# Kernel tuning notes

Measured on AMD Instinct MI355X. Metric: run time of the kernel, lower is better.

Reference implementation:

```python
import jax, jax.numpy as jnp
import numpy as np

# MX microscaling decode helpers. Codes are stored as int32 holding uint8 bit patterns.
_FP4_MAG = jnp.array([0.0, 0.5, 1.0, 1.5, 2.0, 3.0, 4.0, 6.0], dtype=jnp.float32)  # E2M1

def dec_fp4(c):
    # c in [0,16): bit3 = sign, bits0-2 index E2M1 magnitude LUT
    s = jnp.where(c >= 8, -1.0, 1.0)
    return s * _FP4_MAG[c & 7]

def dec_fp6(c):
    # E3M2, bias 3. bit5 sign, bits2-4 exp, bits0-1 mantissa
    s = jnp.where(c >= 32, -1.0, 1.0)
    e = ((c >> 2) & 7).astype(jnp.float32)
    m = (c & 3).astype(jnp.float32)
    mag = jnp.where(e == 0, m * 0.25 * 0.25, (1.0 + m * 0.25) * jnp.exp2(e - 3.0))
    return s * mag

def dec_fp8(c):
    # E4M3, bias 7. bit7 sign, bits3-6 exp, bits0-2 mantissa (NaN code decoded as 480, consistent both sides)
    s = jnp.where(c >= 128, -1.0, 1.0)
    e = ((c >> 3) & 15).astype(jnp.float32)
    m = (c & 7).astype(jnp.float32)
    mag = jnp.where(e == 0, m * 0.125 * jnp.exp2(-6.0), (1.0 + m * 0.125) * jnp.exp2(e - 7.0))
    return s * mag

def unpack4(p):
    # [..., K//2] bytes -> [..., K] nibbles; low nibble = even element, high = odd
    lo = p & 15
    hi = (p >> 4) & 15
    return jnp.stack([lo, hi], axis=-1).reshape(*p.shape[:-1], p.shape[-1] * 2)

def unpack6(p):
    # little-endian 6-bit packing: 4 values per 3 bytes. [..., K*6//8] -> [..., K]
    g = p.reshape(*p.shape[:-1], -1, 3)
    b0, b1, b2 = g[..., 0], g[..., 1], g[..., 2]
    v0 = b0 & 0x3F
    v1 = ((b0 >> 6) & 3) | ((b1 & 0x0F) << 2)
    v2 = ((b1 >> 4) & 0x0F) | ((b2 & 3) << 4)
    v3 = (b2 >> 2) & 0x3F
    return jnp.stack([v0, v1, v2, v3], axis=-1).reshape(*p.shape[:-1], p.shape[-1] * 4 // 3)

def blockscale(x, sf):
    # x [..., K] fp32, sf [..., K//32] E8M0 exponents: scale = 2^(sf-127) per 32-element block
    scale = jnp.exp2(sf.astype(jnp.float32) - 127.0)
    xs = x.reshape(*x.shape[:-1], -1, 32) * scale[..., None]
    return xs.reshape(x.shape)

def dequant(codes, sf, bits):
    if bits == 4:
        x = dec_fp4(unpack4(codes))
    elif bits == 6:
        x = dec_fp6(unpack6(codes))
    else:
        x = dec_fp8(codes)
    return blockscale(x, sf)


def setup_inputs() -> dict:
    key = jax.random.key(0)
    ks = jax.random.split(key, 13)
    M, N = 4096, 4096
    p4, p6, p8 = 3072, 768, 256
    ri = lambda k, sh: jax.random.randint(k, sh, 0, 256, dtype=jnp.int32)
    sf = lambda k, sh: jax.random.randint(k, sh, 121, 132, dtype=jnp.int32)
    return {
        "AN": ri(ks[0], (M, p4 // 2)),
        "AS": ri(ks[1], (M, p6 * 6 // 8)),
        "AO": ri(ks[2], (M, p8)),
        "SFAN": sf(ks[3], (M, p4 // 32)),
        "SFAS": sf(ks[4], (M, p6 // 32)),
        "SFAO": sf(ks[5], (M, p8 // 32)),
        "BN": ri(ks[6], (N, p4 // 2)),
        "BS": ri(ks[7], (N, p6 * 6 // 8)),
        "BO": ri(ks[8], (N, p8)),
        "SFBN": sf(ks[9], (N * p4 // 32,)),
        "SFBS": sf(ks[10], (N * p6 // 32,)),
        "SFBO": sf(ks[11], (N * p8 // 32,)),
        "bias": jax.random.normal(ks[12], (N,), dtype=jnp.float32) * 0.02,
    }


def reference(AN, AS, AO, SFAN, SFAS, SFAO, BN, BS, BO, SFBN, SFBS, SFBO, bias):
    N = BN.shape[0]
    a4 = dequant(AN, SFAN, 4)                       # [M, p4]
    w4 = dequant(BN, SFBN.reshape(N, -1), 4)        # [N, p4]
    a6 = dequant(AS, SFAS, 6)                       # [M, p6]
    w6 = dequant(BS, SFBS.reshape(N, -1), 6)        # [N, p6]
    a8 = dequant(AO, SFAO, 8)                       # [M, p8]
    w8 = dequant(BO, SFBO.reshape(N, -1), 8)        # [N, p8]
    y = a4 @ w4.T + a6 @ w6.T + a8 @ w8.T           # [M, N]
    return y + bias
```

## Files before the change

kernel.cpp:

```cpp
#include <hip/hip_runtime.h>

typedef short short8 __attribute__((ext_vector_type(8)));
typedef int   intx8  __attribute__((ext_vector_type(8)));
typedef float floatx16 __attribute__((ext_vector_type(16)));

__device__ __forceinline__ unsigned pk4(int a, int b, int c, int d) {
    return (a & 255) | ((b & 255) << 8) | ((c & 255) << 16) | ((unsigned)(d & 255) << 24);
}

__device__ __forceinline__ unsigned dec8bf(int c, int esf) {
    int s = (c & 128) << 8;
    int e = (c >> 3) & 15, m = c & 7;
    int rn = s | ((e + 120 + esf) << 7) | (m << 4);
    int nb = (m >= 4) ? 2 : ((m >= 2) ? 1 : 0);
    int rs = m ? (s | ((nb + 118 + esf) << 7) | ((m << (7 - nb)) & 0x7F)) : s;
    return (unsigned)(e ? rn : rs);
}

__global__ __launch_bounds__(256) void pack_lds(
    const int* __restrict__ Pn, const int* __restrict__ Ps, const int* __restrict__ Po,
    const int* __restrict__ Sn, const int* __restrict__ Ss, const int* __restrict__ So,
    unsigned char* __restrict__ C4, unsigned char* __restrict__ C6,
    unsigned short* __restrict__ C8, unsigned char* __restrict__ St, int R)
{
    __shared__ unsigned lds[9216];
    int t = threadIdx.x, b = blockIdx.x, per = R >> 6;
    if (b < 4 * per) {
        int jg = b / per, rb = b - jg * per, r0 = rb << 6;
        #pragma unroll
        for (int i = 0; i < 24; ++i) {
            int idx = i * 256 + t, row = idx / 96, q4 = idx - row * 96;
            int4 v = *(const int4*)(Pn + (size_t)(r0 + row) * 1536 + jg * 384 + q4 * 4);
            lds[row * 96 + q4] = pk4(v.x, v.y, v.z, v.w);
        }
        __syncthreads();
        #pragma unroll
        for (int i = 0; i < 6; ++i) {
            int idx = i * 256 + t, j = idx >> 6, row = idx & 63;
            uint4 v = *(uint4*)&lds[row * 96 + j * 4];
            *(uint4*)(C4 + ((size_t)(jg * 24 + j) * R + r0 + row) * 16) = v;
        }
    } else if (b < 5 * per) {
        int rb = b - 4 * per, r0 = rb << 6;
        #pragma unroll
        for (int i = 0; i < 36; ++i) {
            int idx = i * 256 + t, row = idx / 144, q4 = idx - row * 144;
            int4 v = *(const int4*)(Ps + (size_t)(r0 + row) * 576 + q4 * 4);
            lds[row * 144 + q4] = pk4(v.x, v.y, v.z, v.w);
        }
        __syncthreads();
        #pragma unroll
        for (int i = 0; i < 18; ++i) {
            int idx = i * 256 + t, seg = idx / 192, off = idx - seg * 192;
            int row = off / 3, m3 = off - row * 3;
            int w0 = row * 144 + seg * 6 + m3 * 2;
            int2 v = { (int)lds[w0], (int)lds[w0 + 1] };
            *(int2*)(C6 + ((size_t)seg * R + r0) * 24 + (size_t)off * 8) = v;
        }
    } else if (b < 6 * per) {
        int rb = b - 5 * per, r0 = rb << 6;
        #pragma unroll
        for (int i = 0; i < 16; ++i) {
            int idx = i * 256 + t, row = idx >> 6, q4 = idx & 63;
            int4 c = *(const int4*)(Po + (size_t)(r0 + row) * 256 + q4 * 4);
            int e = So[(size_t)(r0 + row) * 8 + (q4 >> 3)] - 127;
            lds[row * 128 + q4 * 2]     = dec8bf(c.x & 255, e) | (dec8bf(c.y & 255, e) << 16);
            lds[row * 128 + q4 * 2 + 1] = dec8bf(c.z & 255, e) | (dec8bf(c.w & 255, e) << 16);
        }
        __syncthreads();
        #pragma unroll
        for (int i = 0; i < 8; ++i) {
            int idx = i * 256 + t, seg = idx >> 6, row = idx & 63;
            uint4 v = *(uint4*)&lds[row * 128 + seg * 4];
            *(uint4*)((unsigned char*)C8 + ((size_t)seg * R + r0 + row) * 16) = v;
        }
    } else if (b < 7 * per) {
        int rb = b - 6 * per, r0 = rb << 6;
        #pragma unroll
        for (int i = 0; i < 6; ++i) {
            int idx = i * 256 + t, row = idx / 24, q4 = idx - row * 24;
            int4 v = *(const int4*)(Sn + (size_t)(r0 + row) * 96 + q4 * 4);
            lds[row * 24 + q4] = pk4(v.x, v.y, v.z, v.w);
        }
        __syncthreads();
        #pragma unroll
        for (int i = 0; i < 6; ++i) {
            int idx = i * 256 + t, seg = idx >> 6, row = idx & 63;
            *(unsigned*)(St + ((size_t)seg * R + r0 + row) * 4) = lds[row * 24 + seg];
        }
    } else {
        int rb = b - 7 * per, r0 = rb << 6;
        #pragma unroll
        for (int i = 0; i < 3; ++i) {
            int idx = i * 256 + t, row = idx / 12, b2 = idx - row * 12;
            int2 v = *(const int2*)(Ss + (size_t)(r0 + row) * 24 + b2 * 2);
            lds[row * 12 + b2] = (unsigned)((v.x & 255) | ((v.y & 255) << 8));
        }
        __syncthreads();
        #pragma unroll
        for (int i = 0; i < 3; ++i) {
            int idx = i * 256 + t, seg = idx >> 6, row = idx & 63;
            *(unsigned*)(St + ((size_t)(24 + seg) * R + r0 + row) * 4) = lds[row * 12 + seg];
        }
    }
}

__global__ __launch_bounds__(256, 2) void gemm_mx(
    const unsigned char* __restrict__ A4, const unsigned char* __restrict__ B4,
    const unsigned char* __restrict__ A6, const unsigned char* __restrict__ B6,
    const unsigned short* __restrict__ A8, const unsigned short* __restrict__ B8,
    const unsigned char* __restrict__ SaT, const unsigned char* __restrict__ SbT,
    const float* __restrict__ bias, float* __restrict__ C, int M, int N)
{
    int tid = threadIdx.x, w = tid >> 6, l = tid & 63;
    int nbm = M >> 7, nbn = N >> 7;
    int bm, bn;
    if (nbm == 32 && nbn == 32) {
        int o = blockIdx.y * 32 + blockIdx.x;
        int xcd = o & 7, pos = o >> 3;
        int tile = pos >> 4, idx = pos & 15;
        bm = xcd * 4 + (idx & 3);
        bn = tile * 4 + (idx >> 2);
    } else { bm = blockIdx.y; bn = blockIdx.x; }

    int wm = (w >> 1) * 64, wn = (w & 1) * 64;
    int lr = l & 31, lh = l >> 5;

    floatx16 acc[2][2] = {};

    int rA[2] = { bm * 128 + wm + lr, bm * 128 + wm + 32 + lr };
    int cB[2] = { bn * 128 + wn + lr, bn * 128 + wn + 32 + lr };

    {
        unsigned strA = 32u * (unsigned)M, strB = 32u * (unsigned)N;
        unsigned fA0 = ((unsigned)lh * M + (unsigned)rA[0]) * 16u;
        unsigned fA1 = ((unsigned)lh * M + (unsigned)rA[1]) * 16u;
        unsigned fB0 = ((unsigned)lh * N + (unsigned)cB[0]) * 16u;
        unsigned fB1 = ((unsigned)lh * N + (unsigned)cB[1]) * 16u;

        int4 pa[4][2], pb[4][2];
        #pragma unroll
        for (int s = 0; s < 4; ++s) {
            pa[s][0] = *(const int4*)(A4 + fA0); pa[s][1] = *(const int4*)(A4 + fA1);
            pb[s][0] = *(const int4*)(B4 + fB0); pb[s][1] = *(const int4*)(B4 + fB1);
            fA0 += strA; fA1 += strA; fB0 += strB; fB1 += strB;
        }

        unsigned sstrA = 4u * (unsigned)M, sstrB = 4u * (unsigned)N;
        unsigned sA0 = (unsigned)rA[0] * 4u, sA1 = (unsigned)rA[1] * 4u;
        unsigned sB0 = (unsigned)cB[0] * 4u, sB1 = (unsigned)cB[1] * 4u;
        unsigned psa[2][2], psb[2][2];
        psa[0][0] = *(const unsigned*)(SaT + sA0);         psa[0][1] = *(const unsigned*)(SaT + sA1);
        psb[0][0] = *(const unsigned*)(SbT + sB0);         psb[0][1] = *(const unsigned*)(SbT + sB1);
        psa[1][0] = *(const unsigned*)(SaT + sA0 + sstrA); psa[1][1] = *(const unsigned*)(SaT + sA1 + sstrA);
        psb[1][0] = *(const unsigned*)(SbT + sB0 + sstrB); psb[1][1] = *(const unsigned*)(SbT + sB1 + sstrB);
        sA0 += 2 * sstrA; sA1 += 2 * sstrA; sB0 += 2 * sstrB; sB1 += 2 * sstrB;

        #pragma unroll 4
        for (int u = 0; u < 48; ++u) {
            int sl = u & 3, wsl = (u >> 1) & 1;
            int sh = 8 * ((u & 1) * 2 + lh);
            int sa0 = (int)((psa[wsl][0] >> sh) & 255), sa1 = (int)((psa[wsl][1] >> sh) & 255);
            int sb0 = (int)((psb[wsl][0] >> sh) & 255), sb1 = (int)((psb[wsl][1] >> sh) & 255);
            intx8 A0 = (intx8){ pa[sl][0].x, pa[sl][0].y, pa[sl][0].z, pa[sl][0].w, 0, 0, 0, 0 };
            intx8 A1 = (intx8){ pa[sl][1].x, pa[sl][1].y, pa[sl][1].z, pa[sl][1].w, 0, 0, 0, 0 };
            intx8 B0 = (intx8){ pb[sl][0].x, pb[sl][0].y, pb[sl][0].z, pb[sl][0].w, 0, 0, 0, 0 };
            intx8 B1 = (intx8){ pb[sl][1].x, pb[sl][1].y, pb[sl][1].z, pb[sl][1].w, 0, 0, 0, 0 };
            acc[0][0] = __builtin_amdgcn_mfma_scale_f32_32x32x64_f8f6f4(A0, B0, acc[0][0], 4, 4, 0, sa0, 0, sb0);
            acc[0][1] = __builtin_amdgcn_mfma_scale_f32_32x32x64_f8f6f4(A0, B1, acc[0][1], 4, 4, 0, sa0, 0, sb1);
            acc[1][0] = __builtin_amdgcn_mfma_scale_f32_32x32x64_f8f6f4(A1, B0, acc[1][0], 4, 4, 0, sa1, 0, sb0);
            acc[1][1] = __builtin_amdgcn_mfma_scale_f32_32x32x64_f8f6f4(A1, B1, acc[1][1], 4, 4, 0, sa1, 0, sb1);
            pa[sl][0] = *(const int4*)(A4 + fA0); pa[sl][1] = *(const int4*)(A4 + fA1);
            pb[sl][0] = *(const int4*)(B4 + fB0); pb[sl][1] = *(const int4*)(B4 + fB1);
            fA0 += strA; fA1 += strA; fB0 += strB; fB1 += strB;
            if (u & 1) {
                psa[wsl][0] = *(const unsigned*)(SaT + sA0); psa[wsl][1] = *(const unsigned*)(SaT + sA1);
                psb[wsl][0] = *(const unsigned*)(SbT + sB0); psb[wsl][1] = *(const unsigned*)(SbT + sB1);
                sA0 += sstrA; sA1 += sstrA; sB0 += sstrB; sB1 += sstrB;
            }
        }
    }

    {
        unsigned str6A = 48u * (unsigned)M, str6B = 48u * (unsigned)N;
        unsigned gA0 = ((unsigned)lh * M + (unsigned)rA[0]) * 24u;
        unsigned gA1 = ((unsigned)lh * M + (unsigned)rA[1]) * 24u;
        unsigned gB0 = ((unsigned)lh * N + (unsigned)cB[0]) * 24u;
        unsigned gB1 = ((unsigned)lh * N + (unsigned)cB[1]) * 24u;
        unsigned ss4A = 4u * (unsigned)M, ss4B = 4u * (unsigned)N;
        unsigned zA0 = (24u * (unsigned)M + (unsigned)rA[0]) * 4u;
        unsigned zA1 = (24u * (unsigned)M + (unsigned)rA[1]) * 4u;
        unsigned zB0 = (24u * (unsigned)N + (unsigned)cB[0]) * 4u;
        unsigned zB1 = (24u * (unsigned)N + (unsigned)cB[1]) * 4u;

        int2 qa[2][2][3], qb[2][2][3];
        unsigned p6a[2][2], p6b[2][2];
        #pragma unroll
        for (int s = 0; s < 2; ++s) {
            const unsigned char *a0 = A6 + gA0, *a1 = A6 + gA1, *b0 = B6 + gB0, *b1 = B6 + gB1;
            qa[s][0][0] = *(const int2*)(a0); qa[s][0][1] = *(const int2*)(a0 + 8); qa[s][0][2] = *(const int2*)(a0 + 16);
            qa[s][1][0] = *(const int2*)(a1); qa[s][1][1] = *(const int2*)(a1 + 8); qa[s][1][2] = *(const int2*)(a1 + 16);
            qb[s][0][0] = *(const int2*)(b0); qb[s][0][1] = *(const int2*)(b0 + 8); qb[s][0][2] = *(const int2*)(b0 + 16);
            qb[s][1][0] = *(const int2*)(b1); qb[s][1][1] = *(const int2*)(b1 + 8); qb[s][1][2] = *(const int2*)(b1 + 16);
            p6a[s][0] = *(const unsigned*)(SaT + zA0); p6a[s][1] = *(const unsigned*)(SaT + zA1);
            p6b[s][0] = *(const unsigned*)(SbT + zB0); p6b[s][1] = *(const unsigned*)(SbT + zB1);
            gA0 += str6A; gA1 += str6A; gB0 += str6B; gB1 += str6B;
            zA0 += ss4A; zA1 += ss4A; zB0 += ss4B; zB1 += ss4B;
        }
        int sh6 = 8 * lh;
        #pragma unroll 2
        for (int v = 0; v < 10; ++v) {
            int sl = v & 1;
            int sa0 = (int)((p6a[sl][0] >> sh6) & 255), sa1 = (int)((p6a[sl][1] >> sh6) & 255);
            int sb0 = (int)((p6b[sl][0] >> sh6) & 255), sb1 = (int)((p6b[sl][1] >> sh6) & 255);
            intx8 A0 = (intx8){ qa[sl][0][0].x, qa[sl][0][0].y, qa[sl][0][1].x, qa[sl][0][1].y, qa[sl][0][2].x, qa[sl][0][2].y, 0, 0 };
            intx8 A1 = (intx8){ qa[sl][1][0].x, qa[sl][1][0].y, qa[sl][1][1].x, qa[sl][1][1].y, qa[sl][1][2].x, qa[sl][1][2].y, 0, 0 };
            intx8 B0 = (intx8){ qb[sl][0][0].x, qb[sl][0][0].y, qb[sl][0][1].x, qb[sl][0][1].y, qb[sl][0][2].x, qb[sl][0][2].y, 0, 0 };
            intx8 B1 = (intx8){ qb[sl][1][0].x, qb[sl][1][0].y, qb[sl][1][1].x, qb[sl][1][1].y, qb[sl][1][2].x, qb[sl][1][2].y, 0, 0 };
            acc[0][0] = __builtin_amdgcn_mfma_scale_f32_32x32x64_f8f6f4(A0, B0, acc[0][0], 3, 3, 0, sa0, 0, sb0);
            acc[0][1] = __builtin_amdgcn_mfma_scale_f32_32x32x64_f8f6f4(A0, B1, acc[0][1], 3, 3, 0, sa0, 0, sb1);
            acc[1][0] = __builtin_amdgcn_mfma_scale_f32_32x32x64_f8f6f4(A1, B0, acc[1][0], 3, 3, 0, sa1, 0, sb0);
            acc[1][1] = __builtin_amdgcn_mfma_scale_f32_32x32x64_f8f6f4(A1, B1, acc[1][1], 3, 3, 0, sa1, 0, sb1);
            {
                const unsigned char *a0 = A6 + gA0, *a1 = A6 + gA1, *b0 = B6 + gB0, *b1 = B6 + gB1;
                qa[sl][0][0] = *(const int2*)(a0); qa[sl][0][1] = *(const int2*)(a0 + 8); qa[sl][0][2] = *(const int2*)(a0 + 16);
                qa[sl][1][0] = *(const int2*)(a1); qa[sl][1][1] = *(const int2*)(a1 + 8); qa[sl][1][2] = *(const int2*)(a1 + 16);
                qb[sl][0][0] = *(const int2*)(b0); qb[sl][0][1] = *(const int2*)(b0 + 8); qb[sl][0][2] = *(const int2*)(b0 + 16);
                qb[sl][1][0] = *(const int2*)(b1); qb[sl][1][1] = *(const int2*)(b1 + 8); qb[sl][1][2] = *(const int2*)(b1 + 16);
                p6a[sl][0] = *(const unsigned*)(SaT + zA0); p6a[sl][1] = *(const unsigned*)(SaT + zA1);
                p6b[sl][0] = *(const unsigned*)(SbT + zB0); p6b[sl][1] = *(const unsigned*)(SbT + zB1);
                gA0 += str6A; gA1 += str6A; gB0 += str6B; gB1 += str6B;
                zA0 += ss4A; zA1 += ss4A; zB0 += ss4B; zB1 += ss4B;
            }
        }
        #pragma unroll
        for (int v = 10; v < 12; ++v) {
            int sl = v & 1;
            int sa0 = (int)((p6a[sl][0] >> sh6) & 255), sa1 = (int)((p6a[sl][1] >> sh6) & 255);
            int sb0 = (int)((p6b[sl][0] >> sh6) & 255), sb1 = (int)((p6b[sl][1] >> sh6) & 255);
            intx8 A0 = (intx8){ qa[sl][0][0].x, qa[sl][0][0].y, qa[sl][0][1].x, qa[sl][0][1].y, qa[sl][0][2].x, qa[sl][0][2].y, 0, 0 };
            intx8 A1 = (intx8){ qa[sl][1][0].x, qa[sl][1][0].y, qa[sl][1][1].x, qa[sl][1][1].y, qa[sl][1][2].x, qa[sl][1][2].y, 0, 0 };
            intx8 B0 = (intx8){ qb[sl][0][0].x, qb[sl][0][0].y, qb[sl][0][1].x, qb[sl][0][1].y, qb[sl][0][2].x, qb[sl][0][2].y, 0, 0 };
            intx8 B1 = (intx8){ qb[sl][1][0].x, qb[sl][1][0].y, qb[sl][1][1].x, qb[sl][1][1].y, qb[sl][1][2].x, qb[sl][1][2].y, 0, 0 };
            acc[0][0] = __builtin_amdgcn_mfma_scale_f32_32x32x64_f8f6f4(A0, B0, acc[0][0], 3, 3, 0, sa0, 0, sb0);
            acc[0][1] = __builtin_amdgcn_mfma_scale_f32_32x32x64_f8f6f4(A0, B1, acc[0][1], 3, 3, 0, sa0, 0, sb1);
            acc[1][0] = __builtin_amdgcn_mfma_scale_f32_32x32x64_f8f6f4(A1, B0, acc[1][0], 3, 3, 0, sa1, 0, sb0);
            acc[1][1] = __builtin_amdgcn_mfma_scale_f32_32x32x64_f8f6f4(A1, B1, acc[1][1], 3, 3, 0, sa1, 0, sb1);
        }
    }

    {
        unsigned str8A = 32u * (unsigned)M, str8B = 32u * (unsigned)N;
        const unsigned char* A8b = (const unsigned char*)A8;
        const unsigned char* B8b = (const unsigned char*)B8;
        unsigned hA0 = ((unsigned)lh * M + (unsigned)rA[0]) * 16u;
        unsigned hA1 = ((unsigned)lh * M + (unsigned)rA[1]) * 16u;
        unsigned hB0 = ((unsigned)lh * N + (unsigned)cB[0]) * 16u;
        unsigned hB1 = ((unsigned)lh * N + (unsigned)cB[1]) * 16u;
        short8 ra[2][2], rb[2][2];
        #pragma unroll
        for (int s = 0; s < 2; ++s) {
            ra[s][0] = *(const short8*)(A8b + hA0); ra[s][1] = *(const short8*)(A8b + hA1);
            rb[s][0] = *(const short8*)(B8b + hB0); rb[s][1] = *(const short8*)(B8b + hB1);
            hA0 += str8A; hA1 += str8A; hB0 += str8B; hB1 += str8B;
        }
        #pragma unroll 2
        for (int q = 0; q < 16; ++q) {
            int sl = q & 1;
            acc[0][0] = __builtin_amdgcn_mfma_f32_32x32x16_bf16(ra[sl][0], rb[sl][0], acc[0][0], 0, 0, 0);
            acc[0][1] = __builtin_amdgcn_mfma_f32_32x32x16_bf16(ra[sl][0], rb[sl][1], acc[0][1], 0, 0, 0);
            acc[1][0] = __builtin_amdgcn_mfma_f32_32x32x16_bf16(ra[sl][1], rb[sl][0], acc[1][0], 0, 0, 0);
            acc[1][1] = __builtin_amdgcn_mfma_f32_32x32x16_bf16(ra[sl][1], rb[sl][1], acc[1][1], 0, 0, 0);
            ra[sl][0] = *(const short8*)(A8b + hA0); ra[sl][1] = *(const short8*)(A8b + hA1);
            rb[sl][0] = *(const short8*)(B8b + hB0); rb[sl][1] = *(const short8*)(B8b + hB1);
            hA0 += str8A; hA1 += str8A; hB0 += str8B; hB1 += str8B;
        }
    }

    #pragma unroll
    for (int i = 0; i < 2; i++)
        #pragma unroll
        for (int j = 0; j < 2; j++) {
            int col = bn * 128 + wn + j * 32 + lr;
            float bv = bias[col];
            #pragma unroll
            for (int r = 0; r < 16; r++) {
                int row = bm * 128 + wm + i * 32 + (r & 3) + 8 * (r >> 2) + 4 * lh;
                C[(size_t)row * N + col] = acc[i][j][r] + bv;
            }
        }
}

extern "C" void kernel_launch(void* const* d_in, const int* in_sizes, int n_in,
                              void* d_out, int out_size, void* d_ws, size_t ws_size,
                              hipStream_t stream) {
    const int* AN   = (const int*)d_in[0];
    const int* ASs  = (const int*)d_in[1];
    const int* AO   = (const int*)d_in[2];
    const int* SFAN = (const int*)d_in[3];
    const int* SFAS = (const int*)d_in[4];
    const int* SFAO = (const int*)d_in[5];
    const int* BN   = (const int*)d_in[6];
    const int* BS   = (const int*)d_in[7];
    const int* BO   = (const int*)d_in[8];
    const int* SFBN = (const int*)d_in[9];
    const int* SFBS = (const int*)d_in[10];
    const int* SFBO = (const int*)d_in[11];
    const float* bias = (const float*)d_in[12];

    int M = in_sizes[0] / 1536;
    int N = in_sizes[6] / 1536;

    unsigned char* ws = (unsigned char*)d_ws;
    size_t o = 0;
    unsigned char*  A4c = ws + o;                    o += (size_t)M * 1536;
    unsigned char*  B4c = ws + o;                    o += (size_t)N * 1536;
    unsigned char*  A6c = ws + o;                    o += (size_t)M * 576;
    unsigned char*  B6c = ws + o;                    o += (size_t)N * 576;
    unsigned short* A8d = (unsigned short*)(ws + o); o += (size_t)M * 512;
    unsigned short* B8d = (unsigned short*)(ws + o); o += (size_t)N * 512;
    unsigned char*  SaT = ws + o;                    o += (size_t)36 * M * 4;
    unsigned char*  SbT = ws + o;                    o += (size_t)36 * N * 4;

    pack_lds<<<(M >> 6) * 8, 256, 0, stream>>>(AN, ASs, AO, SFAN, SFAS, SFAO,
                                               A4c, A6c, A8d, SaT, M);
    pack_lds<<<(N >> 6) * 8, 256, 0, stream>>>(BN, BS, BO, SFBN, SFBS, SFBO,
                                               B4c, B6c, B8d, SbT, N);

    dim3 grid(N / 128, M / 128);
    gemm_mx<<<grid, 256, 0, stream>>>(A4c, B4c, A6c, B6c, A8d, B8d,
                                      SaT, SbT, bias, (float*)d_out, M, N);
}
```

Baseline: 220.1 us.

## Stage FP4 operand tiles through LDS with direct global-to-LDS loads

The FP4 phase now fetches A and B fragments with global_load_lds into a 4-slot LDS ring, then reads them back per wave after a barrier. Before, each wave loaded its fragments straight into registers. The change cuts register pressure so occupancy can rise to 3 blocks per CU, and lets the two waves sharing rows or columns reuse one fetch. It also removes the XCD-aware tile swizzle and goes back to plain blockIdx mapping, which may hurt L2 locality. A barrier per K-step and hand-tuned vmcnt waits are added, and the vmcnt counts must also cover the interleaved scale loads.

```diff
diff --git a/kernel.cpp b/kernel.cpp
--- a/kernel.cpp
+++ b/kernel.cpp
@@ -3,6 +3,12 @@
 typedef short short8 __attribute__((ext_vector_type(8)));
 typedef int   intx8  __attribute__((ext_vector_type(8)));
 typedef float floatx16 __attribute__((ext_vector_type(16)));
+
+typedef const __attribute__((address_space(1))) void* gas_t;
+typedef __attribute__((address_space(3))) void* las_t;
+__device__ __forceinline__ void gload16(const void* g, void* l) {
+    __builtin_amdgcn_global_load_lds((gas_t)g, (las_t)l, 16, 0, 0);
+}
 
 __device__ __forceinline__ unsigned pk4(int a, int b, int c, int d) {
     return (a & 255) | ((b & 255) << 8) | ((c & 255) << 16) | ((unsigned)(d & 255) << 24);
@@ -105,24 +111,17 @@
     }
 }
 
-__global__ __launch_bounds__(256, 2) void gemm_mx(
+__global__ __launch_bounds__(256, 3) void gemm_mx(
     const unsigned char* __restrict__ A4, const unsigned char* __restrict__ B4,
     const unsigned char* __restrict__ A6, const unsigned char* __restrict__ B6,
     const unsigned short* __restrict__ A8, const unsigned short* __restrict__ B8,
     const unsigned char* __restrict__ SaT, const unsigned char* __restrict__ SbT,
     const float* __restrict__ bias, float* __restrict__ C, int M, int N)
 {
+    __shared__ int4 ldsm[2048];
+    char* ldsb = (char*)ldsm;
     int tid = threadIdx.x, w = tid >> 6, l = tid & 63;
-    int nbm = M >> 7, nbn = N >> 7;
-    int bm, bn;
-    if (nbm == 32 && nbn == 32) {
-        int o = blockIdx.y * 32 + blockIdx.x;
-        int xcd = o & 7, pos = o >> 3;
-        int tile = pos >> 4, idx = pos & 15;
-        bm = xcd * 4 + (idx & 3);
-        bn = tile * 4 + (idx >> 2);
-    } else { bm = blockIdx.y; bn = blockIdx.x; }
-
+    int bm = blockIdx.y, bn = blockIdx.x;
     int wm = (w >> 1) * 64, wn = (w & 1) * 64;
     int lr = l & 31, lh = l >> 5;
 
@@ -133,18 +132,12 @@
 
     {
         unsigned strA = 32u * (unsigned)M, strB = 32u * (unsigned)N;
-        unsigned fA0 = ((unsigned)lh * M + (unsigned)rA[0]) * 16u;
-        unsigned fA1 = ((unsigned)lh * M + (unsigned)rA[1]) * 16u;
-        unsigned fB0 = ((unsigned)lh * N + (unsigned)cB[0]) * 16u;
-        unsigned fB1 = ((unsigned)lh * N + (unsigned)cB[1]) * 16u;
-
-        int4 pa[4][2], pb[4][2];
-        #pragma unroll
-        for (int s = 0; s < 4; ++s) {
-            pa[s][0] = *(const int4*)(A4 + fA0); pa[s][1] = *(const int4*)(A4 + fA1);
-            pb[s][0] = *(const int4*)(B4 + fB0); pb[s][1] = *(const int4*)(B4 + fB1);
-            fA0 += strA; fA1 += strA; fB0 += strB; fB1 += strB;
-        }
+        unsigned gA = ((unsigned)(w >> 1) * (unsigned)M + (unsigned)(bm * 128 + (w & 1) * 64 + l)) * 16u;
+        unsigned gB = ((unsigned)(w >> 1) * (unsigned)N + (unsigned)(bn * 128 + (w & 1) * 64 + l)) * 16u;
+        char* lw = ldsb + w * 1024;
+        gload16(A4 + gA, lw);                 gload16(B4 + gB, lw + 4096);
+        gload16(A4 + gA + strA, lw + 8192);   gload16(B4 + gB + strB, lw + 8192 + 4096);
+        gA += 2 * strA; gB += 2 * strB;
 
         unsigned sstrA = 4u * (unsigned)M, sstrB = 4u * (unsigned)N;
         unsigned sA0 = (unsigned)rA[0] * 4u, sA1 = (unsigned)rA[1] * 4u;
@@ -156,29 +149,44 @@
         psb[1][0] = *(const unsigned*)(SbT + sB0 + sstrB); psb[1][1] = *(const unsigned*)(SbT + sB1 + sstrB);
         sA0 += 2 * sstrA; sA1 += 2 * sstrA; sB0 += 2 * sstrB; sB1 += 2 * sstrB;
 
-        #pragma unroll 4
-        for (int u = 0; u < 48; ++u) {
-            int sl = u & 3, wsl = (u >> 1) & 1;
-            int sh = 8 * ((u & 1) * 2 + lh);
-            int sa0 = (int)((psa[wsl][0] >> sh) & 255), sa1 = (int)((psa[wsl][1] >> sh) & 255);
-            int sb0 = (int)((psb[wsl][0] >> sh) & 255), sb1 = (int)((psb[wsl][1] >> sh) & 255);
-            intx8 A0 = (intx8){ pa[sl][0].x, pa[sl][0].y, pa[sl][0].z, pa[sl][0].w, 0, 0, 0, 0 };
-            intx8 A1 = (intx8){ pa[sl][1].x, pa[sl][1].y, pa[sl][1].z, pa[sl][1].w, 0, 0, 0, 0 };
-            intx8 B0 = (intx8){ pb[sl][0].x, pb[sl][0].y, pb[sl][0].z, pb[sl][0].w, 0, 0, 0, 0 };
-            intx8 B1 = (intx8){ pb[sl][1].x, pb[sl][1].y, pb[sl][1].z, pb[sl][1].w, 0, 0, 0, 0 };
-            acc[0][0] = __builtin_amdgcn_mfma_scale_f32_32x32x64_f8f6f4(A0, B0, acc[0][0], 4, 4, 0, sa0, 0, sb0);
-            acc[0][1] = __builtin_amdgcn_mfma_scale_f32_32x32x64_f8f6f4(A0, B1, acc[0][1], 4, 4, 0, sa0, 0, sb1);
-            acc[1][0] = __builtin_amdgcn_mfma_scale_f32_32x32x64_f8f6f4(A1, B0, acc[1][0], 4, 4, 0, sa1, 0, sb0);
-            acc[1][1] = __builtin_amdgcn_mfma_scale_f32_32x32x64_f8f6f4(A1, B1, acc[1][1], 4, 4, 0, sa1, 0, sb1);
-            pa[sl][0] = *(const int4*)(A4 + fA0); pa[sl][1] = *(const int4*)(A4 + fA1);
-            pb[sl][0] = *(const int4*)(B4 + fB0); pb[sl][1] = *(const int4*)(B4 + fB1);
-            fA0 += strA; fA1 += strA; fB0 += strB; fB1 += strB;
-            if (u & 1) {
-                psa[wsl][0] = *(const unsigned*)(SaT + sA0); psa[wsl][1] = *(const unsigned*)(SaT + sA1);
-                psb[wsl][0] = *(const unsigned*)(SbT + sB0); psb[wsl][1] = *(const unsigned*)(SbT + sB1);
-                sA0 += sstrA; sA1 += sstrA; sB0 += sstrB; sB1 += sstrB;
-            }
-        }
+        const int aof = (lh << 11) + ((wm + lr) << 4);
+        const int bof = 4096 + (lh << 11) + ((wn + lr) << 4);
+
+#define FP4_STEP(K4)                                                                   \
+        {                                                                              \
+            gload16(A4 + gA, ldsb + (((K4) + 2) & 3) * 8192 + w * 1024);               \
+            gload16(B4 + gB, ldsb + (((K4) + 2) & 3) * 8192 + 4096 + w * 1024);        \
+            gA += strA; gB += strB;                                                    \
+            asm volatile("s_waitcnt vmcnt(%0)" :: "i"(((K4) & 1) ? 4 : 8) : "memory"); \
+            __builtin_amdgcn_s_barrier();                                              \
+            const char* lb = ldsb + (K4) * 8192;                                       \
+            int4 va0 = *(const int4*)(lb + aof), va1 = *(const int4*)(lb + aof + 512); \
+            int4 vb0 = *(const int4*)(lb + bof), vb1 = *(const int4*)(lb + bof + 512); \
+            int sh = 8 * (((K4) & 1) * 2 + lh);                                        \
+            int sa0 = (int)((psa[((K4) >> 1) & 1][0] >> sh) & 255);                    \
+            int sa1 = (int)((psa[((K4) >> 1) & 1][1] >> sh) & 255);                    \
+            int sb0 = (int)((psb[((K4) >> 1) & 1][0] >> sh) & 255);                    \
+            int sb1 = (int)((psb[((K4) >> 1) & 1][1] >> sh) & 255);                    \
+            intx8 A0 = (intx8){ va0.x, va0.y, va0.z, va0.w, 0, 0, 0, 0 };              \
+            intx8 A1 = (intx8){ va1.x, va1.y, va1.z, va1.w, 0, 0, 0, 0 };              \
+            intx8 B0 = (intx8){ vb0.x, vb0.y, vb0.z, vb0.w, 0, 0, 0, 0 };              \
+            intx8 B1 = (intx8){ vb1.x, vb1.y, vb1.z, vb1.w, 0, 0, 0, 0 };              \
+            acc[0][0] = __builtin_amdgcn_mfma_scale_f32_32x32x64_f8f6f4(A0, B0, acc[0][0], 4, 4, 0, sa0, 0, sb0); \
+            acc[0][1] = __builtin_amdgcn_mfma_scale_f32_32x32x64_f8f6f4(A0, B1, acc[0][1], 4, 4, 0, sa0, 0, sb1); \
+            acc[1][0] = __builtin_amdgcn_mfma_scale_f32_32x32x64_f8f6f4(A1, B0, acc[1][0], 4, 4, 0, sa1, 0, sb0); \
+            acc[1][1] = __builtin_amdgcn_mfma_scale_f32_32x32x64_f8f6f4(A1, B1, acc[1][1], 4, 4, 0, sa1, 0, sb1); \
+            if ((K4) & 1) {                                                            \
+                int W = ((K4) >> 1) & 1;                                               \
+                psa[W][0] = *(const unsigned*)(SaT + sA0); psa[W][1] = *(const unsigned*)(SaT + sA1); \
+                psb[W][0] = *(const unsigned*)(SbT + sB0); psb[W][1] = *(const unsigned*)(SbT + sB1); \
+                sA0 += sstrA; sA1 += sstrA; sB0 += sstrB; sB1 += sstrB;                \
+            }                                                                          \
+        }
+
+        for (int uu = 0; uu < 12; ++uu) {
+            FP4_STEP(0) FP4_STEP(1) FP4_STEP(2) FP4_STEP(3)
+        }
+#undef FP4_STEP
     }
 
     {
```

Result: slower. 229.1 us (+4.1%).

## Widen block tile to 128x256 with 2x4 MFMA tiles per wave

Applied to the files above, without the earlier changes.

Each wave now computes a 64x128 output tile (2x4 MFMA accumulators) instead of 64x64, and the block tile grows to 128x256, halving the grid along N. A fragments are reused across four B columns, which cuts redundant global loads per MFMA. The XCD-aware block swizzle is removed, and the FP4 prefetch depth drops from 4 to 3 stages to save registers. This raises register pressure with 8 accumulators and launch_bounds(256,2), which may cause spills or lower occupancy, and the grid shrinks to 512 blocks.

```diff
diff --git a/kernel.cpp b/kernel.cpp
--- a/kernel.cpp
+++ b/kernel.cpp
@@ -113,139 +113,182 @@
     const float* __restrict__ bias, float* __restrict__ C, int M, int N)
 {
     int tid = threadIdx.x, w = tid >> 6, l = tid & 63;
-    int nbm = M >> 7, nbn = N >> 7;
-    int bm, bn;
-    if (nbm == 32 && nbn == 32) {
-        int o = blockIdx.y * 32 + blockIdx.x;
-        int xcd = o & 7, pos = o >> 3;
-        int tile = pos >> 4, idx = pos & 15;
-        bm = xcd * 4 + (idx & 3);
-        bn = tile * 4 + (idx >> 2);
-    } else { bm = blockIdx.y; bn = blockIdx.x; }
-
-    int wm = (w >> 1) * 64, wn = (w & 1) * 64;
+    int bm = blockIdx.y, bn = blockIdx.x;
+    int wm = (w >> 1) * 64, wn = (w & 1) * 128;
     int lr = l & 31, lh = l >> 5;
 
-    floatx16 acc[2][2] = {};
-
-    int rA[2] = { bm * 128 + wm + lr, bm * 128 + wm + 32 + lr };
-    int cB[2] = { bn * 128 + wn + lr, bn * 128 + wn + 32 + lr };
+    floatx16 acc[2][4] = {};
+
+    int rA[2], cB[4];
+    #pragma unroll
+    for (int i = 0; i < 2; ++i) rA[i] = bm * 128 + wm + i * 32 + lr;
+    #pragma unroll
+    for (int j = 0; j < 4; ++j) cB[j] = bn * 256 + wn + j * 32 + lr;
 
     {
         unsigned strA = 32u * (unsigned)M, strB = 32u * (unsigned)N;
-        unsigned fA0 = ((unsigned)lh * M + (unsigned)rA[0]) * 16u;
-        unsigned fA1 = ((unsigned)lh * M + (unsigned)rA[1]) * 16u;
-        unsigned fB0 = ((unsigned)lh * N + (unsigned)cB[0]) * 16u;
-        unsigned fB1 = ((unsigned)lh * N + (unsigned)cB[1]) * 16u;
-
-        int4 pa[4][2], pb[4][2];
-        #pragma unroll
-        for (int s = 0; s < 4; ++s) {
-            pa[s][0] = *(const int4*)(A4 + fA0); pa[s][1] = *(const int4*)(A4 + fA1);
-            pb[s][0] = *(const int4*)(B4 + fB0); pb[s][1] = *(const int4*)(B4 + fB1);
-            fA0 += strA; fA1 += strA; fB0 += strB; fB1 += strB;
+        unsigned fA[2], fB[4];
+        #pragma unroll
+        for (int i = 0; i < 2; ++i) fA[i] = ((unsigned)lh * M + (unsigned)rA[i]) * 16u;
+        #pragma unroll
+        for (int j = 0; j < 4; ++j) fB[j] = ((unsigned)lh * N + (unsigned)cB[j]) * 16u;
+
+        int4 pa[3][2], pb[3][4];
+        #pragma unroll
+        for (int s = 0; s < 3; ++s) {
+            #pragma unroll
+            for (int i = 0; i < 2; ++i) { pa[s][i] = *(const int4*)(A4 + fA[i]); fA[i] += strA; }
+            #pragma unroll
+            for (int j = 0; j < 4; ++j) { pb[s][j] = *(const int4*)(B4 + fB[j]); fB[j] += strB; }
         }
 
         unsigned sstrA = 4u * (unsigned)M, sstrB = 4u * (unsigned)N;
-        unsigned sA0 = (unsigned)rA[0] * 4u, sA1 = (unsigned)rA[1] * 4u;
-        unsigned sB0 = (unsigned)cB[0] * 4u, sB1 = (unsigned)cB[1] * 4u;
-        unsigned psa[2][2], psb[2][2];
-        psa[0][0] = *(const unsigned*)(SaT + sA0);         psa[0][1] = *(const unsigned*)(SaT + sA1);
-        psb[0][0] = *(const unsigned*)(SbT + sB0);         psb[0][1] = *(const unsigned*)(SbT + sB1);
-        psa[1][0] = *(const unsigned*)(SaT + sA0 + sstrA); psa[1][1] = *(const unsigned*)(SaT + sA1 + sstrA);
-        psb[1][0] = *(const unsigned*)(SbT + sB0 + sstrB); psb[1][1] = *(const unsigned*)(SbT + sB1 + sstrB);
-        sA0 += 2 * sstrA; sA1 += 2 * sstrA; sB0 += 2 * sstrB; sB1 += 2 * sstrB;
-
-        #pragma unroll 4
+        unsigned sA[2], sB[4];
+        unsigned psa[2][2], psb[2][4];
+        #pragma unroll
+        for (int i = 0; i < 2; ++i) {
+            sA[i] = (unsigned)rA[i] * 4u;
+            psa[0][i] = *(const unsigned*)(SaT + sA[i]);
+            psa[1][i] = *(const unsigned*)(SaT + sA[i] + sstrA);
+            sA[i] += 2 * sstrA;
+        }
+        #pragma unroll
+        for (int j = 0; j < 4; ++j) {
+            sB[j] = (unsigned)cB[j] * 4u;
+            psb[0][j] = *(const unsigned*)(SbT + sB[j]);
+            psb[1][j] = *(const unsigned*)(SbT + sB[j] + sstrB);
+            sB[j] += 2 * sstrB;
+        }
+
+        #pragma unroll 12
         for (int u = 0; u < 48; ++u) {
-            int sl = u & 3, wsl = (u >> 1) & 1;
+            int sl = u % 3, wsl = (u >> 1) & 1;
             int sh = 8 * ((u & 1) * 2 + lh);
-            int sa0 = (int)((psa[wsl][0] >> sh) & 255), sa1 = (int)((psa[wsl][1] >> sh) & 255);
-            int sb0 = (int)((psb[wsl][0] >> sh) & 255), sb1 = (int)((psb[wsl][1] >> sh) & 255);
-            intx8 A0 = (intx8){ pa[sl][0].x, pa[sl][0].y, pa[sl][0].z, pa[sl][0].w, 0, 0, 0, 0 };
-            intx8 A1 = (intx8){ pa[sl][1].x, pa[sl][1].y, pa[sl][1].z, pa[sl][1].w, 0, 0, 0, 0 };
-            intx8 B0 = (intx8){ pb[sl][0].x, pb[sl][0].y, pb[sl][0].z, pb[sl][0].w, 0, 0, 0, 0 };
-            intx8 B1 = (intx8){ pb[sl][1].x, pb[sl][1].y, pb[sl][1].z, pb[sl][1].w, 0, 0, 0, 0 };
-            acc[0][0] = __builtin_amdgcn_mfma_scale_f32_32x32x64_f8f6f4(A0, B0, acc[0][0], 4, 4, 0, sa0, 0, sb0);
-            acc[0][1] = __builtin_amdgcn_mfma_scale_f32_32x32x64_f8f6f4(A0, B1, acc[0][1], 4, 4, 0, sa0, 0, sb1);
-            acc[1][0] = __builtin_amdgcn_mfma_scale_f32_32x32x64_f8f6f4(A1, B0, acc[1][0], 4, 4, 0, sa1, 0, sb0);
-            acc[1][1] = __builtin_amdgcn_mfma_scale_f32_32x32x64_f8f6f4(A1, B1, acc[1][1], 4, 4, 0, sa1, 0, sb1);
-            pa[sl][0] = *(const int4*)(A4 + fA0); pa[sl][1] = *(const int4*)(A4 + fA1);
-            pb[sl][0] = *(const int4*)(B4 + fB0); pb[sl][1] = *(const int4*)(B4 + fB1);
-            fA0 += strA; fA1 += strA; fB0 += strB; fB1 += strB;
+            int sa[2], sb[4];
+            #pragma unroll
+            for (int i = 0; i < 2; ++i) sa[i] = (int)((psa[wsl][i] >> sh) & 255);
+            #pragma unroll
+            for (int j = 0; j < 4; ++j) sb[j] = (int)((psb[wsl][j] >> sh) & 255);
+            intx8 Afr[2], Bfr[4];
+            #pragma unroll
+            for (int i = 0; i < 2; ++i)
+                Afr[i] = (intx8){ pa[sl][i].x, pa[sl][i].y, pa[sl][i].z, pa[sl][i].w, 0, 0, 0, 0 };
+            #pragma unroll
+            for (int j = 0; j < 4; ++j)
+                Bfr[j] = (intx8){ pb[sl][j].x, pb[sl][j].y, pb[sl][j].z, pb[sl][j].w, 0, 0, 0, 0 };
+            #pragma unroll
+            for (int i = 0; i < 2; ++i)
+                #pragma unroll
+                for (int j = 0; j < 4; ++j)
+                    acc[i][j] = __builtin_amdgcn_mfma_scale_f32_32x32x64_f8f6f4(
+                        Afr[i], Bfr[j], acc[i][j], 4, 4, 0, sa[i], 0, sb[j]);
+            #pragma unroll
+            for (int i = 0; i < 2; ++i) { pa[sl][i] = *(const int4*)(A4 + fA[i]); fA[i] += strA; }
+            #pragma unroll
+            for (int j = 0; j < 4; ++j) { pb[sl][j] = *(const int4*)(B4 + fB[j]); fB[j] += strB; }
             if (u & 1) {
-                psa[wsl][0] = *(const unsigned*)(SaT + sA0); psa[wsl][1] = *(const unsigned*)(SaT + sA1);
-                psb[wsl][0] = *(const unsigned*)(SbT + sB0); psb[wsl][1] = *(const unsigned*)(SbT + sB1);
-                sA0 += sstrA; sA1 += sstrA; sB0 += sstrB; sB1 += sstrB;
+                #pragma unroll
+                for (int i = 0; i < 2; ++i) { psa[wsl][i] = *(const unsigned*)(SaT + sA[i]); sA[i] += sstrA; }
+                #pragma unroll
+                for (int j = 0; j < 4; ++j) { psb[wsl][j] = *(const unsigned*)(SbT + sB[j]); sB[j] += sstrB; }
             }
         }
     }
 
     {
         unsigned str6A = 48u * (unsigned)M, str6B = 48u * (unsigned)N;
-        unsigned gA0 = ((unsigned)lh * M + (unsigned)rA[0]) * 24u;
-        unsigned gA1 = ((unsigned)lh * M + (unsigned)rA[1]) * 24u;
-        unsigned gB0 = ((unsigned)lh * N + (unsigned)cB[0]) * 24u;
-        unsigned gB1 = ((unsigned)lh * N + (unsigned)cB[1]) * 24u;
         unsigned ss4A = 4u * (unsigned)M, ss4B = 4u * (unsigned)N;
-        unsigned zA0 = (24u * (unsigned)M + (unsigned)rA[0]) * 4u;
-        unsigned zA1 = (24u * (unsigned)M + (unsigned)rA[1]) * 4u;
-        unsigned zB0 = (24u * (unsigned)N + (unsigned)cB[0]) * 4u;
-        unsigned zB1 = (24u * (unsigned)N + (unsigned)cB[1]) * 4u;
-
-        int2 qa[2][2][3], qb[2][2][3];
-        unsigned p6a[2][2], p6b[2][2];
+        unsigned gA[2], gB[4], zA[2], zB[4];
+        #pragma unroll
+        for (int i = 0; i < 2; ++i) {
+            gA[i] = ((unsigned)lh * M + (unsigned)rA[i]) * 24u;
+            zA[i] = (24u * (unsigned)M + (unsigned)rA[i]) * 4u;
+        }
+        #pragma unroll
+        for (int j = 0; j < 4; ++j) {
+            gB[j] = ((unsigned)lh * N + (unsigned)cB[j]) * 24u;
+            zB[j] = (24u * (unsigned)N + (unsigned)cB[j]) * 4u;
+        }
+
+        int2 qa[2][2][3], qb[2][4][3];
+        unsigned p6a[2][2], p6b[2][4];
         #pragma unroll
         for (int s = 0; s < 2; ++s) {
-            const unsigned char *a0 = A6 + gA0, *a1 = A6 + gA1, *b0 = B6 + gB0, *b1 = B6 + gB1;
-            qa[s][0][0] = *(const int2*)(a0); qa[s][0][1] = *(const int2*)(a0 + 8); qa[s][0][2] = *(const int2*)(a0 + 16);
-            qa[s][1][0] = *(const int2*)(a1); qa[s][1][1] = *(const int2*)(a1 + 8); qa[s][1][2] = *(const int2*)(a1 + 16);
-            qb[s][0][0] = *(const int2*)(b0); qb[s][0][1] = *(const int2*)(b0 + 8); qb[s][0][2] = *(const int2*)(b0 + 16);
-            qb[s][1][0] = *(const int2*)(b1); qb[s][1][1] = *(const int2*)(b1 + 8); qb[s][1][2] = *(const int2*)(b1 + 16);
-            p6a[s][0] = *(const unsigned*)(SaT + zA0); p6a[s][1] = *(const unsigned*)(SaT + zA1);
-            p6b[s][0] = *(const unsigned*)(SbT + zB0); p6b[s][1] = *(const unsigned*)(SbT + zB1);
-            gA0 += str6A; gA1 += str6A; gB0 += str6B; gB1 += str6B;
-            zA0 += ss4A; zA1 += ss4A; zB0 += ss4B; zB1 += ss4B;
+            #pragma unroll
+            for (int i = 0; i < 2; ++i) {
+                const unsigned char* p = A6 + gA[i];
+                qa[s][i][0] = *(const int2*)(p); qa[s][i][1] = *(const int2*)(p + 8); qa[s][i][2] = *(const int2*)(p + 16);
+                p6a[s][i] = *(const unsigned*)(SaT + zA[i]);
+                gA[i] += str6A; zA[i] += ss4A;
+            }
+            #pragma unroll
+            for (int j = 0; j < 4; ++j) {
+                const unsigned char* p = B6 + gB[j];
+                qb[s][j][0] = *(const int2*)(p); qb[s][j][1] = *(const int2*)(p + 8); qb[s][j][2] = *(const int2*)(p + 16);
+                p6b[s][j] = *(const unsigned*)(SbT + zB[j]);
+                gB[j] += str6B; zB[j] += ss4B;
+            }
         }
         int sh6 = 8 * lh;
         #pragma unroll 2
         for (int v = 0; v < 10; ++v) {
             int sl = v & 1;
-            int sa0 = (int)((p6a[sl][0] >> sh6) & 255), sa1 = (int)((p6a[sl][1] >> sh6) & 255);
-            int sb0 = (int)((p6b[sl][0] >> sh6) & 255), sb1 = (int)((p6b[sl][1] >> sh6) & 255);
-            intx8 A0 = (intx8){ qa[sl][0][0].x, qa[sl][0][0].y, qa[sl][0][1].x, qa[sl][0][1].y, qa[sl][0][2].x, qa[sl][0][2].y, 0, 0 };
-            intx8 A1 = (intx8){ qa[sl][1][0].x, qa[sl][1][0].y, qa[sl][1][1].x, qa[sl][1][1].y, qa[sl][1][2].x, qa[sl][1][2].y, 0, 0 };
-            intx8 B0 = (intx8){ qb[sl][0][0].x, qb[sl][0][0].y, qb[sl][0][1].x, qb[sl][0][1].y, qb[sl][0][2].x, qb[sl][0][2].y, 0, 0 };
-            intx8 B1 = (intx8){ qb[sl][1][0].x, qb[sl][1][0].y, qb[sl][1][1].x, qb[sl][1][1].y, qb[sl][1][2].x, qb[sl][1][2].y, 0, 0 };
-            acc[0][0] = __builtin_amdgcn_mfma_scale_f32_32x32x64_f8f6f4(A0, B0, acc[0][0], 3, 3, 0, sa0, 0, sb0);
-            acc[0][1] = __builtin_amdgcn_mfma_scale_f32_32x32x64_f8f6f4(A0, B1, acc[0][1], 3, 3, 0, sa0, 0, sb1);
-            acc[1][0] = __builtin_amdgcn_mfma_scale_f32_32x32x64_f8f6f4(A1, B0, acc[1][0], 3, 3, 0, sa1, 0, sb0);
-            acc[1][1] = __builtin_amdgcn_mfma_scale_f32_32x32x64_f8f6f4(A1, B1, acc[1][1], 3, 3, 0, sa1, 0, sb1);
+            int sa[2], sb[4];
+            #pragma unroll
+            for (int i = 0; i < 2; ++i) sa[i] = (int)((p6a[sl][i] >> sh6) & 255);
+            #pragma unroll
+            for (int j = 0; j < 4; ++j) sb[j] = (int)((p6b[sl][j] >> sh6) & 255);
+            intx8 Afr[2], Bfr[4];
+            #pragma unroll
+            for (int i = 0; i < 2; ++i)
+                Afr[i] = (intx8){ qa[sl][i][0].x, qa[sl][i][0].y, qa[sl][i][1].x, qa[sl][i][1].y, qa[sl][i][2].x, qa[sl][i][2].y, 0, 0 };
+            #pragma unroll
+            for (int j = 0; j < 4; ++j)
+                Bfr[j] = (intx8){ qb[sl][j][0].x, qb[sl][j][0].y, qb[sl][j][1].x, qb[sl][j][1].y, qb[sl][j][2].x, qb[sl][j][2].y, 0, 0 };
+            #pragma unroll
+            for (int i = 0; i < 2; ++i)
+                #pragma unroll
+                for (int j = 0; j < 4; ++j)
+                    acc[i][j] = __builtin_amdgcn_mfma_scale_f32_32x32x64_f8f6f4(
+                        Afr[i], Bfr[j], acc[i][j], 3, 3, 0, sa[i], 0, sb[j]);
             {
-                const unsigned char *a0 = A6 + gA0, *a1 = A6 + gA1, *b0 = B6 + gB0, *b1 = B6 + gB1;
-                qa[sl][0][0] = *(const int2*)(a0); qa[sl][0][1] = *(const int2*)(a0 + 8); qa[sl][0][2] = *(const int2*)(a0 + 16);
-                qa[sl][1][0] = *(const int2*)(a1); qa[sl][1][1] = *(const int2*)(a1 + 8); qa[sl][1][2] = *(const int2*)(a1 + 16);
-                qb[sl][0][0] = *(const int2*)(b0); qb[sl][0][1] = *(const int2*)(b0 + 8); qb[sl][0][2] = *(const int2*)(b0 + 16);
-                qb[sl][1][0] = *(const int2*)(b1); qb[sl][1][1] = *(const int2*)(b1 + 8); qb[sl][1][2] = *(const int2*)(b1 + 16);
-                p6a[sl][0] = *(const unsigned*)(SaT + zA0); p6a[sl][1] = *(const unsigned*)(SaT + zA1);
-                p6b[sl][0] = *(const unsigned*)(SbT + zB0); p6b[sl][1] = *(const unsigned*)(SbT + zB1);
-                gA0 += str6A; gA1 += str6A; gB0 += str6B; gB1 += str6B;
-                zA0 += ss4A; zA1 += ss4A; zB0 += ss4B; zB1 += ss4B;
+                #pragma unroll
+                for (int i = 0; i < 2; ++i) {
+                    const unsigned char* p = A6 + gA[i];
+                    qa[sl][i][0] = *(const int2*)(p); qa[sl][i][1] = *(const int2*)(p + 8); qa[sl][i][2] = *(const int2*)(p + 16);
+                    p6a[sl][i] = *(const unsigned*)(SaT + zA[i]);
+                    gA[i] += str6A; zA[i] += ss4A;
+                }
+                #pragma unroll
+                for (int j = 0; j < 4; ++j) {
+                    const unsigned char* p = B6 + gB[j];
+                    qb[sl][j][0] = *(const int2*)(p); qb[sl][j][1] = *(const int2*)(p + 8); qb[sl][j][2] = *(const int2*)(p + 16);
+                    p6b[sl][j] = *(const unsigned*)(SbT + zB[j]);
+                    gB[j] += str6B; zB[j] += ss4B;
+                }
             }
         }
         #pragma unroll
         for (int v = 10; v < 12; ++v) {
             int sl = v & 1;
-            int sa0 = (int)((p6a[sl][0] >> sh6) & 255), sa1 = (int)((p6a[sl][1] >> sh6) & 255);
-            int sb0 = (int)((p6b[sl][0] >> sh6) & 255), sb1 = (int)((p6b[sl][1] >> sh6) & 255);
-            intx8 A0 = (intx8){ qa[sl][0][0].x, qa[sl][0][0].y, qa[sl][0][1].x, qa[sl][0][1].y, qa[sl][0][2].x, qa[sl][0][2].y, 0, 0 };
-            intx8 A1 = (intx8){ qa[sl][1][0].x, qa[sl][1][0].y, qa[sl][1][1].x, qa[sl][1][1].y, qa[sl][1][2].x, qa[sl][1][2].y, 0, 0 };
-            intx8 B0 = (intx8){ qb[sl][0][0].x, qb[sl][0][0].y, qb[sl][0][1].x, qb[sl][0][1].y, qb[sl][0][2].x, qb[sl][0][2].y, 0, 0 };
-            intx8 B1 = (intx8){ qb[sl][1][0].x, qb[sl][1][0].y, qb[sl][1][1].x, qb[sl][1][1].y, qb[sl][1][2].x, qb[sl][1][2].y, 0, 0 };
-            acc[0][0] = __builtin_amdgcn_mfma_scale_f32_32x32x64_f8f6f4(A0, B0, acc[0][0], 3, 3, 0, sa0, 0, sb0);
-            acc[0][1] = __builtin_amdgcn_mfma_scale_f32_32x32x64_f8f6f4(A0, B1, acc[0][1], 3, 3, 0, sa0, 0, sb1);
-            acc[1][0] = __builtin_amdgcn_mfma_scale_f32_32x32x64_f8f6f4(A1, B0, acc[1][0], 3, 3, 0, sa1, 0, sb0);
-            acc[1][1] = __builtin_amdgcn_mfma_scale_f32_32x32x64_f8f6f4(A1, B1, acc[1][1], 3, 3, 0, sa1, 0, sb1);
+            int sa[2], sb[4];
+            #pragma unroll
+            for (int i = 0; i < 2; ++i) sa[i] = (int)((p6a[sl][i] >> sh6) & 255);
+            #pragma unroll
+            for (int j = 0; j < 4; ++j) sb[j] = (int)((p6b[sl][j] >> sh6) & 255);
+            intx8 Afr[2], Bfr[4];
+            #pragma unroll
+            for (int i = 0; i < 2; ++i)
+                Afr[i] = (intx8){ qa[sl][i][0].x, qa[sl][i][0].y, qa[sl][i][1].x, qa[sl][i][1].y, qa[sl][i][2].x, qa[sl][i][2].y, 0, 0 };
+            #pragma unroll
+            for (int j = 0; j < 4; ++j)
+                Bfr[j] = (intx8){ qb[sl][j][0].x, qb[sl][j][0].y, qb[sl][j][1].x, qb[sl][j][1].y, qb[sl][j][2].x, qb[sl][j][2].y, 0, 0 };
+            #pragma unroll
+            for (int i = 0; i < 2; ++i)
+                #pragma unroll
+                for (int j = 0; j < 4; ++j)
+                    acc[i][j] = __builtin_amdgcn_mfma_scale_f32_32x32x64_f8f6f4(
+                        Afr[i], Bfr[j], acc[i][j], 3, 3, 0, sa[i], 0, sb[j]);
         }
     }
 
@@ -253,35 +296,39 @@
         unsigned str8A = 32u * (unsigned)M, str8B = 32u * (unsigned)N;
         const unsigned char* A8b = (const unsigned char*)A8;
         const unsigned char* B8b = (const unsigned char*)B8;
-        unsigned hA0 = ((unsigned)lh * M + (unsigned)rA[0]) * 16u;
-        unsigned hA1 = ((unsigned)lh * M + (unsigned)rA[1]) * 16u;
-        unsigned hB0 = ((unsigned)lh * N + (unsigned)cB[0]) * 16u;
-        unsigned hB1 = ((unsigned)lh * N + (unsigned)cB[1]) * 16u;
-        short8 ra[2][2], rb[2][2];
+        unsigned hA[2], hB[4];
+        #pragma unroll
+        for (int i = 0; i < 2; ++i) hA[i] = ((unsigned)lh * M + (unsigned)rA[i]) * 16u;
+        #pragma unroll
+        for (int j = 0; j < 4; ++j) hB[j] = ((unsigned)lh * N + (unsigned)cB[j]) * 16u;
+        short8 ra[2][2], rb[2][4];
         #pragma unroll
         for (int s = 0; s < 2; ++s) {
-            ra[s][0] = *(const short8*)(A8b + hA0); ra[s][1] = *(const short8*)(A8b + hA1);
-            rb[s][0] = *(const short8*)(B8b + hB0); rb[s][1] = *(const short8*)(B8b + hB1);
-            hA0 += str8A; hA1 += str8A; hB0 += str8B; hB1 += str8B;
+            #pragma unroll
+            for (int i = 0; i < 2; ++i) { ra[s][i] = *(const short8*)(A8b + hA[i]); hA[i] += str8A; }
+            #pragma unroll
+            for (int j = 0; j < 4; ++j) { rb[s][j] = *(const short8*)(B8b + hB[j]); hB[j] += str8B; }
         }
         #pragma unroll 2
         for (int q = 0; q < 16; ++q) {
             int sl = q & 1;
-            acc[0][0] = __builtin_amdgcn_mfma_f32_32x32x16_bf16(ra[sl][0], rb[sl][0], acc[0][0], 0, 0, 0);
-            acc[0][1] = __builtin_amdgcn_mfma_f32_32x32x16_bf16(ra[sl][0], rb[sl][1], acc[0][1], 0, 0, 0);
-            acc[1][0] = __builtin_amdgcn_mfma_f32_32x32x16_bf16(ra[sl][1], rb[sl][0], acc[1][0], 0, 0, 0);
-            acc[1][1] = __builtin_amdgcn_mfma_f32_32x32x16_bf16(ra[sl][1], rb[sl][1], acc[1][1], 0, 0, 0);
-            ra[sl][0] = *(const short8*)(A8b + hA0); ra[sl][1] = *(const short8*)(A8b + hA1);
-            rb[sl][0] = *(const short8*)(B8b + hB0); rb[sl][1] = *(const short8*)(B8b + hB1);
-            hA0 += str8A; hA1 += str8A; hB0 += str8B; hB1 += str8B;
+            #pragma unroll
+            for (int i = 0; i < 2; ++i)
+                #pragma unroll
+                for (int j = 0; j < 4; ++j)
+                    acc[i][j] = __builtin_amdgcn_mfma_f32_32x32x16_bf16(ra[sl][i], rb[sl][j], acc[i][j], 0, 0, 0);
+            #pragma unroll
+            for (int i = 0; i < 2; ++i) { ra[sl][i] = *(const short8*)(A8b + hA[i]); hA[i] += str8A; }
+            #pragma unroll
+            for (int j = 0; j < 4; ++j) { rb[sl][j] = *(const short8*)(B8b + hB[j]); hB[j] += str8B; }
         }
     }
 
     #pragma unroll
     for (int i = 0; i < 2; i++)
         #pragma unroll
-        for (int j = 0; j < 2; j++) {
-            int col = bn * 128 + wn + j * 32 + lr;
+        for (int j = 0; j < 4; j++) {
+            int col = bn * 256 + wn + j * 32 + lr;
             float bv = bias[col];
             #pragma unroll
             for (int r = 0; r < 16; r++) {
@@ -327,7 +374,7 @@
     pack_lds<<<(N >> 6) * 8, 256, 0, stream>>>(BN, BS, BO, SFBN, SFBS, SFBO,
                                                B4c, B6c, B8d, SbT, N);
 
-    dim3 grid(N / 128, M / 128);
+    dim3 grid(N / 256, M / 128);
     gemm_mx<<<grid, 256, 0, stream>>>(A4c, B4c, A6c, B6c, A8d, B8d,
                                       SaT, SbT, bias, (float*)d_out, M, N);
 }
```

Measured after the change: 291.2 us. 32.3% more time.
